# Optimization experiments

Hardware: AMD Instinct MI355X
Metric: run time of the kernel (lower is better)

The kernel has to match this reference:

```python
import jax, jax.numpy as jnp
import numpy as np

N_WIRES = 4
N_LAYERS = 3
N_PATCH = 196  # 14x14 2x2 patches of a 28x28 image


def setup_inputs() -> dict:
    key = jax.random.key(0)
    k1, k2, k3 = jax.random.split(key, 3)
    B = 8192
    x = jax.random.uniform(k1, (B, 28, 28), dtype=jnp.float32)
    theta = jax.random.normal(k2, (N_LAYERS, N_WIRES), dtype=jnp.float32) * 0.1
    W = jax.random.normal(k3, (10, 4 * 14 * 14), dtype=jnp.float32) * 0.02
    b = jnp.zeros((10,), jnp.float32)
    return {"x": x, "theta": theta, "W": W, "b": b}


def _apply_ry(state, theta, wire):
    # state: (B, P, 2, 2, 2, 2); RY(theta) = [[cos t/2, -sin t/2], [sin t/2, cos t/2]]
    ax = 2 + wire
    half = theta * 0.5
    c, s = jnp.cos(half), jnp.sin(half)
    if jnp.ndim(c):  # per-(B,P) encoder angle: broadcast over the 3 remaining wire axes
        c = c[..., None, None, None]
        s = s[..., None, None, None]
    s0 = jax.lax.index_in_dim(state, 0, ax, keepdims=False)
    s1 = jax.lax.index_in_dim(state, 1, ax, keepdims=False)
    return jnp.stack([c * s0 - s * s1, s * s0 + c * s1], axis=ax)


def _quanv(x, theta):
    B = x.shape[0]
    # 2x2 stride-2 patches, row-major over (r, c); within-patch order
    # [x[r,c], x[r,c+1], x[r+1,c], x[r+1,c+1]]
    patches = x.reshape(B, 14, 2, 14, 2).transpose(0, 1, 3, 2, 4).reshape(B, N_PATCH, 4)
    # encoder resets to |0000>; all gates are real RY, so amplitudes stay real
    state = jnp.zeros((B, N_PATCH, 2, 2, 2, 2), x.dtype).at[:, :, 0, 0, 0, 0].set(1.0)
    for w in range(N_WIRES):  # encoder: RY(data_w) on wire w
        state = _apply_ry(state, patches[:, :, w], w)
    for l in range(N_LAYERS):  # variational layers: RY(theta[l,w]) on wire w
        for w in range(N_WIRES):
            state = _apply_ry(state, theta[l, w], w)
    probs = state * state  # (B, P, 2,2,2,2), real amplitudes
    meas = []
    for w in range(N_WIRES):  # <Z_w> = P(wire w = 0) - P(wire w = 1)
        other = tuple(a for a in range(2, 6) if a != 2 + w)
        p = probs.sum(axis=other)  # (B, P, 2)
        meas.append(p[..., 0] - p[..., 1])
    return jnp.stack(meas, axis=-1).reshape(B, N_PATCH * N_WIRES)  # (B, 784)


def reference(x, theta, W, b):
    feats = _quanv(x, theta)            # (B, 784)
    logits = feats @ W.T + b            # (B, 10)
    return jax.nn.log_softmax(logits, axis=-1)
```

## Files before the change

### kernel.cpp

```cpp
#include <hip/hip_runtime.h>
#include <math.h>

#define NPIX 784
#define NCLS 10
#define ROWS_PER_BLOCK 16

__global__ void quanv_prep_kernel(const float* __restrict__ theta,
                                  const float* __restrict__ W,
                                  float* __restrict__ Wp,
                                  float* __restrict__ Tq) {
    __shared__ float Tsum[4];
    int tid = threadIdx.x;
    if (tid < 4) Tsum[tid] = theta[tid] + theta[4 + tid] + theta[8 + tid];
    __syncthreads();
    for (int idx = tid; idx < NCLS * NPIX; idx += blockDim.x) {
        int k = idx / NPIX;
        int q = idx - k * NPIX;
        int i = q / 28, j = q - i * 28;
        int f = (((i >> 1) * 14 + (j >> 1)) << 2) + ((i & 1) * 2 + (j & 1));
        Wp[idx] = W[k * NPIX + f];
    }
    for (int q = tid; q < NPIX; q += blockDim.x) {
        int i = q / 28, j = q - i * 28;
        Tq[q] = Tsum[(i & 1) * 2 + (j & 1)];
    }
}

__global__ __launch_bounds__(256)
void quanv_main_kernel(const float* __restrict__ x,
                       const float* __restrict__ Wp,
                       const float* __restrict__ Tq,
                       const float* __restrict__ bias,
                       float* __restrict__ out, int B) {
    __shared__ float Wl[NCLS * NPIX];
    __shared__ float Tl[NPIX];
    int tid = threadIdx.x;
    for (int idx = tid; idx < NCLS * NPIX; idx += 256) Wl[idx] = Wp[idx];
    for (int idx = tid; idx < NPIX; idx += 256) Tl[idx] = Tq[idx];
    __syncthreads();

    int tx = tid & 15;
    int row = blockIdx.x * ROWS_PER_BLOCK + (tid >> 4);

    float acc[NCLS];
#pragma unroll
    for (int k = 0; k < NCLS; ++k) acc[k] = 0.f;

    if (row < B) {
        const float* xr = x + (size_t)row * NPIX;
#pragma unroll
        for (int s = 0; s < 13; ++s) {
            int p = (tx + (s << 4)) << 2;
            if (p < NPIX) {
                float4 xv = *reinterpret_cast<const float4*>(xr + p);
                float4 tv = *reinterpret_cast<const float4*>(&Tl[p]);
                float f0 = __cosf(xv.x + tv.x);
                float f1 = __cosf(xv.y + tv.y);
                float f2 = __cosf(xv.z + tv.z);
                float f3 = __cosf(xv.w + tv.w);
#pragma unroll
                for (int k = 0; k < NCLS; ++k) {
                    float4 wv = *reinterpret_cast<const float4*>(&Wl[k * NPIX + p]);
                    acc[k] += f0 * wv.x + f1 * wv.y + f2 * wv.z + f3 * wv.w;
                }
            }
        }
    }

#pragma unroll
    for (int k = 0; k < NCLS; ++k) {
        float v = acc[k];
        v += __shfl_xor(v, 1);
        v += __shfl_xor(v, 2);
        v += __shfl_xor(v, 4);
        v += __shfl_xor(v, 8);
        acc[k] = v;
    }

    if (tx == 0 && row < B) {
        float logits[NCLS];
        float m = -1e30f;
#pragma unroll
        for (int k = 0; k < NCLS; ++k) {
            logits[k] = acc[k] + bias[k];
            m = fmaxf(m, logits[k]);
        }
        float sum = 0.f;
#pragma unroll
        for (int k = 0; k < NCLS; ++k) sum += expf(logits[k] - m);
        float lse = m + logf(sum);
#pragma unroll
        for (int k = 0; k < NCLS; ++k) out[row * NCLS + k] = logits[k] - lse;
    }
}

extern "C" void kernel_launch(void* const* d_in, const int* in_sizes, int n_in,
                              void* d_out, int out_size, void* d_ws, size_t ws_size,
                              hipStream_t stream) {
    const float* x     = (const float*)d_in[0];
    const float* theta = (const float*)d_in[1];
    const float* W     = (const float*)d_in[2];
    const float* bias  = (const float*)d_in[3];
    float* out = (float*)d_out;

    float* Wp = (float*)d_ws;
    float* Tq = Wp + NCLS * NPIX;

    int B = in_sizes[0] / NPIX;

    quanv_prep_kernel<<<1, 256, 0, stream>>>(theta, W, Wp, Tq);
    int grid = (B + ROWS_PER_BLOCK - 1) / ROWS_PER_BLOCK;
    quanv_main_kernel<<<grid, 256, 0, stream>>>(x, Wp, Tq, bias, out, B);
}
```

Measured before the change: 92.16 us.

## Fuse weight permutation into main kernel and use 32 lanes per row

Removes the single-block prep kernel by having every block load W with float4 reads and scatter it into the pixel-ordered shared layout itself, and computes the theta sums inline. The main loop now assigns 32 lanes per row (8 rows per block) instead of 16, with a tail step for the remaining 4 float4s, and drops the row bounds check by assuming B divisible by 8. This removes a serialized launch and the workspace round trip, but doubles the number of blocks that each reload the full 31 KB weight table into LDS.

```diff
diff --git a/kernel.cpp b/kernel.cpp
--- a/kernel.cpp
+++ b/kernel.cpp
@@ -3,67 +3,80 @@
 
 #define NPIX 784
 #define NCLS 10
-#define ROWS_PER_BLOCK 16
-
-__global__ void quanv_prep_kernel(const float* __restrict__ theta,
-                                  const float* __restrict__ W,
-                                  float* __restrict__ Wp,
-                                  float* __restrict__ Tq) {
-    __shared__ float Tsum[4];
-    int tid = threadIdx.x;
-    if (tid < 4) Tsum[tid] = theta[tid] + theta[4 + tid] + theta[8 + tid];
-    __syncthreads();
-    for (int idx = tid; idx < NCLS * NPIX; idx += blockDim.x) {
-        int k = idx / NPIX;
-        int q = idx - k * NPIX;
-        int i = q / 28, j = q - i * 28;
-        int f = (((i >> 1) * 14 + (j >> 1)) << 2) + ((i & 1) * 2 + (j & 1));
-        Wp[idx] = W[k * NPIX + f];
-    }
-    for (int q = tid; q < NPIX; q += blockDim.x) {
-        int i = q / 28, j = q - i * 28;
-        Tq[q] = Tsum[(i & 1) * 2 + (j & 1)];
-    }
-}
+#define ROWS 8
+#define LPR 32
+#define BLOCK 256
 
 __global__ __launch_bounds__(256)
-void quanv_main_kernel(const float* __restrict__ x,
-                       const float* __restrict__ Wp,
-                       const float* __restrict__ Tq,
-                       const float* __restrict__ bias,
-                       float* __restrict__ out, int B) {
+void quanv_fused_kernel(const float* __restrict__ x,
+                        const float* __restrict__ theta,
+                        const float* __restrict__ W,
+                        const float* __restrict__ bias,
+                        float* __restrict__ out) {
     __shared__ float Wl[NCLS * NPIX];
     __shared__ float Tl[NPIX];
     int tid = threadIdx.x;
-    for (int idx = tid; idx < NCLS * NPIX; idx += 256) Wl[idx] = Wp[idx];
-    for (int idx = tid; idx < NPIX; idx += 256) Tl[idx] = Tq[idx];
+
+    for (int idx4 = tid; idx4 < (NCLS * NPIX) / 4; idx4 += BLOCK) {
+        float4 wv = reinterpret_cast<const float4*>(W)[idx4];
+        int idx = idx4 << 2;
+        int k = idx / NPIX;
+        int p = idx - k * NPIX;
+        int patch = p >> 2;
+        int pr = patch / 14, pc = patch - pr * 14;
+        int q0 = (pr * 28 + pc) * 2;
+        float* dst = &Wl[k * NPIX + q0];
+        dst[0]  = wv.x;  dst[1]  = wv.y;
+        dst[28] = wv.z;  dst[29] = wv.w;
+    }
+    float t0 = theta[0] + theta[4] + theta[8];
+    float t1 = theta[1] + theta[5] + theta[9];
+    float t2 = theta[2] + theta[6] + theta[10];
+    float t3 = theta[3] + theta[7] + theta[11];
+    for (int q = tid; q < NPIX; q += BLOCK) {
+        int i = q / 28;
+        int j = q - i * 28;
+        float ta = (i & 1) ? t2 : t0;
+        float tb = (i & 1) ? t3 : t1;
+        Tl[q] = (j & 1) ? tb : ta;
+    }
     __syncthreads();
 
-    int tx = tid & 15;
-    int row = blockIdx.x * ROWS_PER_BLOCK + (tid >> 4);
+    int tx = tid & (LPR - 1);
+    int row = blockIdx.x * ROWS + (tid >> 5);
+    const float* xr = x + (size_t)row * NPIX;
 
     float acc[NCLS];
 #pragma unroll
     for (int k = 0; k < NCLS; ++k) acc[k] = 0.f;
 
-    if (row < B) {
-        const float* xr = x + (size_t)row * NPIX;
 #pragma unroll
-        for (int s = 0; s < 13; ++s) {
-            int p = (tx + (s << 4)) << 2;
-            if (p < NPIX) {
-                float4 xv = *reinterpret_cast<const float4*>(xr + p);
-                float4 tv = *reinterpret_cast<const float4*>(&Tl[p]);
-                float f0 = __cosf(xv.x + tv.x);
-                float f1 = __cosf(xv.y + tv.y);
-                float f2 = __cosf(xv.z + tv.z);
-                float f3 = __cosf(xv.w + tv.w);
+    for (int s = 0; s < 6; ++s) {
+        int p = (tx + (s << 5)) << 2;
+        float4 xv = *reinterpret_cast<const float4*>(xr + p);
+        float4 tv = *reinterpret_cast<const float4*>(&Tl[p]);
+        float f0 = __cosf(xv.x + tv.x);
+        float f1 = __cosf(xv.y + tv.y);
+        float f2 = __cosf(xv.z + tv.z);
+        float f3 = __cosf(xv.w + tv.w);
 #pragma unroll
-                for (int k = 0; k < NCLS; ++k) {
-                    float4 wv = *reinterpret_cast<const float4*>(&Wl[k * NPIX + p]);
-                    acc[k] += f0 * wv.x + f1 * wv.y + f2 * wv.z + f3 * wv.w;
-                }
-            }
+        for (int k = 0; k < NCLS; ++k) {
+            float4 wv = *reinterpret_cast<const float4*>(&Wl[k * NPIX + p]);
+            acc[k] += f0 * wv.x + f1 * wv.y + f2 * wv.z + f3 * wv.w;
+        }
+    }
+    if (tx < 4) {
+        int p = (tx + 192) << 2;
+        float4 xv = *reinterpret_cast<const float4*>(xr + p);
+        float4 tv = *reinterpret_cast<const float4*>(&Tl[p]);
+        float f0 = __cosf(xv.x + tv.x);
+        float f1 = __cosf(xv.y + tv.y);
+        float f2 = __cosf(xv.z + tv.z);
+        float f3 = __cosf(xv.w + tv.w);
+#pragma unroll
+        for (int k = 0; k < NCLS; ++k) {
+            float4 wv = *reinterpret_cast<const float4*>(&Wl[k * NPIX + p]);
+            acc[k] += f0 * wv.x + f1 * wv.y + f2 * wv.z + f3 * wv.w;
         }
     }
 
@@ -74,10 +87,11 @@
         v += __shfl_xor(v, 2);
         v += __shfl_xor(v, 4);
         v += __shfl_xor(v, 8);
+        v += __shfl_xor(v, 16);
         acc[k] = v;
     }
 
-    if (tx == 0 && row < B) {
+    if (tx == 0) {
         float logits[NCLS];
         float m = -1e30f;
 #pragma unroll
@@ -103,12 +117,7 @@
     const float* bias  = (const float*)d_in[3];
     float* out = (float*)d_out;
 
-    float* Wp = (float*)d_ws;
-    float* Tq = Wp + NCLS * NPIX;
-
     int B = in_sizes[0] / NPIX;
-
-    quanv_prep_kernel<<<1, 256, 0, stream>>>(theta, W, Wp, Tq);
-    int grid = (B + ROWS_PER_BLOCK - 1) / ROWS_PER_BLOCK;
-    quanv_main_kernel<<<grid, 256, 0, stream>>>(x, Wp, Tq, bias, out, B);
+    int grid = B / ROWS;
+    quanv_fused_kernel<<<grid, BLOCK, 0, stream>>>(x, theta, W, bias, out);
 }
```

Result: faster. 80.88 us (-12.2%).
